# Kernel optimization log

Hardware: AMD Instinct MI355X
Metric: run time of the kernel (lower is better)

The kernel has to match this reference:

```python
import jax, jax.numpy as jnp
import numpy as np

B, T, D = 2, 2048, 2048
H = 16
NOPE, ROPE = 128, 64
Q_HEAD = NOPE + ROPE            # 192
Q_LORA = H * Q_HEAD // 4        # 768
KV_RANK = 512
V_DIM = 128
EPS = 1e-6


def setup_inputs() -> dict:
    key = jax.random.key(0)
    ks = jax.random.split(key, 8)
    s = lambda k, shape: jax.random.normal(k, shape, dtype=jnp.float32) * (1.0 / np.sqrt(shape[0]))
    return {
        "hidden_states": jax.random.normal(ks[0], (B, T, D), dtype=jnp.float32),
        "positions": jnp.broadcast_to(jnp.arange(T, dtype=jnp.int64 if jax.config.jax_enable_x64 else jnp.int32), (B, T)),
        "w_qa": s(ks[1], (D, Q_LORA)),
        "g_qa": jnp.ones((Q_LORA,), jnp.float32),
        "w_qb": s(ks[2], (Q_LORA, H * Q_HEAD)),
        "w_kva": s(ks[3], (D, KV_RANK + ROPE)),
        "g_kva": jnp.ones((KV_RANK,), jnp.float32),
        "w_kvb": s(ks[4], (KV_RANK, H * (NOPE + V_DIM))),
        "w_o": s(ks[5], (H * V_DIM, D)),
    }


def _rms(x, g):
    return x * jax.lax.rsqrt(jnp.mean(x * x, axis=-1, keepdims=True) + EPS) * g


def _rotate_half(x):
    h = x.shape[-1] // 2
    return jnp.concatenate([-x[..., h:], x[..., :h]], axis=-1)


def _rope_tables(n):
    inv_freq = 1.0 / (10000.0 ** (jnp.arange(0, ROPE, 2, dtype=jnp.float32) / ROPE))
    freqs = jnp.arange(n, dtype=jnp.float32)[:, None] * inv_freq[None, :]
    emb = jnp.concatenate([freqs, freqs], axis=-1)  # [n, ROPE]
    return jnp.cos(emb), jnp.sin(emb)


def reference(hidden_states, positions, w_qa, g_qa, w_qb, w_kva, g_kva, w_kvb, w_o):
    Bq, Tq, _ = hidden_states.shape
    # Q: low-rank down-proj + RMSNorm + up-proj
    q = _rms(hidden_states @ w_qa, g_qa) @ w_qb
    q = q.reshape(Bq, Tq, H, Q_HEAD)
    q_nope, q_rope = q[..., :NOPE], q[..., NOPE:]
    # KV compression (prefill: no past cache, S == T)
    kvc = hidden_states @ w_kva
    new_c_kv = _rms(kvc[..., :KV_RANK], g_kva)     # [B,S,rank]
    new_k_rope = kvc[..., KV_RANK:]                # [B,S,ROPE]
    S = new_c_kv.shape[1]
    kv = (new_c_kv @ w_kvb).reshape(Bq, S, H, NOPE + V_DIM)
    k_nope, v = kv[..., :NOPE], kv[..., NOPE:]
    # Decoupled RoPE on the rope sub-dimension only
    cos_full, sin_full = _rope_tables(S)
    cos_q = cos_full[positions][:, :, None, :]     # [B,T,1,ROPE]
    sin_q = sin_full[positions][:, :, None, :]
    q_rope = q_rope * cos_q + _rotate_half(q_rope) * sin_q
    cos_k = cos_full[None, :, :]                   # [1,S,ROPE] (all_positions = arange(S))
    sin_k = sin_full[None, :, :]
    k_rope = new_k_rope * cos_k + _rotate_half(new_k_rope) * sin_k  # [B,S,ROPE], shared across heads
    # Assemble full q/k, attention
    q_full = jnp.concatenate([q_nope, q_rope], axis=-1).transpose(0, 2, 1, 3)  # [B,H,T,192]
    k_full = jnp.concatenate(
        [k_nope, jnp.broadcast_to(k_rope[:, :, None, :], (Bq, S, H, ROPE))], axis=-1
    ).transpose(0, 2, 1, 3)                                                     # [B,H,S,192]
    v = v.transpose(0, 2, 1, 3)                                                 # [B,H,S,Vd]
    scale = Q_HEAD ** -0.5
    attn = jnp.einsum("bhtd,bhsd->bhts", q_full, k_full) * scale
    row = jnp.arange(Tq)[:, None]
    col = jnp.arange(S)[None, :]
    attn = jnp.where(col > row + (S - Tq), -jnp.inf, attn)
    attn = jax.nn.softmax(attn, axis=-1)
    out = jnp.einsum("bhts,bhsd->bhtd", attn, v)
    out = out.transpose(0, 2, 1, 3).reshape(Bq, Tq, H * V_DIM)
    output = out @ w_o
    return output, new_c_kv, new_k_rope
```

## Files before the change

kernel.cpp:

```cpp
#include <hip/hip_runtime.h>
#include <stdint.h>

typedef unsigned short ushort_t;
typedef ushort_t u16x8 __attribute__((ext_vector_type(8)));
typedef short s16x8 __attribute__((ext_vector_type(8)));
typedef float f32x4 __attribute__((ext_vector_type(4)));

#define B_ 2
#define T_ 2048
#define D_ 2048
#define H_ 16
#define NOPE_ 128
#define ROPE_ 64
#define QHEAD_ 192
#define QLORA_ 768
#define KVRANK_ 512
#define VDIM_ 128
#define MROWS (B_*T_)
#define QKVW 1408

#define MAGIC_F32  0x3F800000u
#define MAGIC_BF16 0x3F803F80u

#define QK_SCALE 0.07216878364870323f

__device__ __forceinline__ float bf2f(ushort_t u) {
    return __uint_as_float(((uint32_t)u) << 16);
}
__device__ __forceinline__ ushort_t f2bf(float f) {
    uint32_t x = __float_as_uint(f);
    x += 0x7fffu + ((x >> 16) & 1u);
    return (ushort_t)(x >> 16);
}

__device__ __forceinline__ void async_ld16(const ushort_t* g, ushort_t* l) {
    __builtin_amdgcn_global_load_lds(
        (const __attribute__((address_space(1))) void*)g,
        (__attribute__((address_space(3))) void*)l, 16, 0, 0);
}

__launch_bounds__(256)
__global__ void gemm_mfma(const ushort_t* __restrict__ A,
                          const ushort_t* __restrict__ BT,
                          float* __restrict__ C, int M, int N, int K) {
    __shared__ ushort_t As[128 * 32];
    __shared__ ushort_t Bs[128 * 32];

    const int tid = threadIdx.x;
    const int lane = tid & 63;
    const int n16 = lane & 15, quad = lane >> 4;
    const int m0 = blockIdx.y * 128, n0 = blockIdx.x * 128;
    const int w = tid >> 6;
    const int wm = (w & 1) * 64, wn = (w >> 1) * 64;

    f32x4 acc[4][4];
#pragma unroll
    for (int i = 0; i < 4; i++)
#pragma unroll
        for (int j = 0; j < 4; j++) acc[i][j] = (f32x4){0.f, 0.f, 0.f, 0.f};

    const int wbase = tid & ~63;
    for (int kt = 0; kt < K; kt += 32) {
        __syncthreads();
#pragma unroll
        for (int iss = 0; iss < 2; iss++) {
            const int chunk = iss * 256 + tid;
            const int row = chunk >> 2, col = (chunk & 3) * 8;
            const int lbase = (iss * 256 + wbase) * 8;
            async_ld16(A + (long)(m0 + row) * K + kt + col, &As[lbase]);
            async_ld16(BT + (long)(n0 + row) * K + kt + col, &Bs[lbase]);
        }
        __syncthreads();

        s16x8 af[4], bf[4];
#pragma unroll
        for (int i = 0; i < 4; i++) {
            af[i] = *(const s16x8*)&As[(wm + i * 16 + n16) * 32 + quad * 8];
            bf[i] = *(const s16x8*)&Bs[(wn + i * 16 + n16) * 32 + quad * 8];
        }
#pragma unroll
        for (int i = 0; i < 4; i++)
#pragma unroll
            for (int j = 0; j < 4; j++)
                acc[i][j] = __builtin_amdgcn_mfma_f32_16x16x32_bf16(af[i], bf[j], acc[i][j], 0, 0, 0);
    }

#pragma unroll
    for (int i = 0; i < 4; i++) {
        const long mrow = m0 + wm + i * 16 + quad * 4;
#pragma unroll
        for (int j = 0; j < 4; j++) {
            const int nc = n0 + wn + j * 16 + n16;
#pragma unroll
            for (int r = 0; r < 4; r++)
                C[(mrow + r) * N + nc] = acc[i][j][r];
        }
    }
}

__launch_bounds__(256)
__global__ void gemm_mfma_h(const ushort_t* __restrict__ A,
                            const ushort_t* __restrict__ BT,
                            ushort_t* __restrict__ C, int M, int N, int K) {
    __shared__ ushort_t As[128 * 32];
    __shared__ ushort_t Bs[128 * 32];

    const int tid = threadIdx.x;
    const int lane = tid & 63;
    const int n16 = lane & 15, quad = lane >> 4;
    const int m0 = blockIdx.y * 128, n0 = blockIdx.x * 128;
    const int w = tid >> 6;
    const int wm = (w & 1) * 64, wn = (w >> 1) * 64;

    f32x4 acc[4][4];
#pragma unroll
    for (int i = 0; i < 4; i++)
#pragma unroll
        for (int j = 0; j < 4; j++) acc[i][j] = (f32x4){0.f, 0.f, 0.f, 0.f};

    const int wbase = tid & ~63;
    for (int kt = 0; kt < K; kt += 32) {
        __syncthreads();
#pragma unroll
        for (int iss = 0; iss < 2; iss++) {
            const int chunk = iss * 256 + tid;
            const int row = chunk >> 2, col = (chunk & 3) * 8;
            const int lbase = (iss * 256 + wbase) * 8;
            async_ld16(A + (long)(m0 + row) * K + kt + col, &As[lbase]);
            async_ld16(BT + (long)(n0 + row) * K + kt + col, &Bs[lbase]);
        }
        __syncthreads();

        s16x8 af[4], bf[4];
#pragma unroll
        for (int i = 0; i < 4; i++) {
            af[i] = *(const s16x8*)&As[(wm + i * 16 + n16) * 32 + quad * 8];
            bf[i] = *(const s16x8*)&Bs[(wn + i * 16 + n16) * 32 + quad * 8];
        }
#pragma unroll
        for (int i = 0; i < 4; i++)
#pragma unroll
            for (int j = 0; j < 4; j++)
                acc[i][j] = __builtin_amdgcn_mfma_f32_16x16x32_bf16(af[i], bf[j], acc[i][j], 0, 0, 0);
    }

#pragma unroll
    for (int i = 0; i < 4; i++) {
        const long mrow = m0 + wm + i * 16 + quad * 4;
#pragma unroll
        for (int j = 0; j < 4; j++) {
            const int nc = n0 + wn + j * 16 + n16;
#pragma unroll
            for (int r = 0; r < 4; r++)
                C[(mrow + r) * N + nc] = f2bf(acc[i][j][r]);
        }
    }
}

__launch_bounds__(256)
__global__ void gemm_out_k(const uint32_t* __restrict__ probe,
                           const ushort_t* __restrict__ A,
                           const ushort_t* __restrict__ BT,
                           float* __restrict__ Cf, ushort_t* __restrict__ Ch,
                           int M, int N, int K) {
    __shared__ ushort_t As[128 * 32];
    __shared__ ushort_t Bs[128 * 32];

    const bool isf = (*probe == MAGIC_F32);
    const int tid = threadIdx.x;
    const int lane = tid & 63;
    const int n16 = lane & 15, quad = lane >> 4;
    const int m0 = blockIdx.y * 128, n0 = blockIdx.x * 128;
    const int w = tid >> 6;
    const int wm = (w & 1) * 64, wn = (w >> 1) * 64;

    f32x4 acc[4][4];
#pragma unroll
    for (int i = 0; i < 4; i++)
#pragma unroll
        for (int j = 0; j < 4; j++) acc[i][j] = (f32x4){0.f, 0.f, 0.f, 0.f};

    const int wbase = tid & ~63;
    for (int kt = 0; kt < K; kt += 32) {
        __syncthreads();
#pragma unroll
        for (int iss = 0; iss < 2; iss++) {
            const int chunk = iss * 256 + tid;
            const int row = chunk >> 2, col = (chunk & 3) * 8;
            const int lbase = (iss * 256 + wbase) * 8;
            async_ld16(A + (long)(m0 + row) * K + kt + col, &As[lbase]);
            async_ld16(BT + (long)(n0 + row) * K + kt + col, &Bs[lbase]);
        }
        __syncthreads();

        s16x8 af[4], bf[4];
#pragma unroll
        for (int i = 0; i < 4; i++) {
            af[i] = *(const s16x8*)&As[(wm + i * 16 + n16) * 32 + quad * 8];
            bf[i] = *(const s16x8*)&Bs[(wn + i * 16 + n16) * 32 + quad * 8];
        }
#pragma unroll
        for (int i = 0; i < 4; i++)
#pragma unroll
            for (int j = 0; j < 4; j++)
                acc[i][j] = __builtin_amdgcn_mfma_f32_16x16x32_bf16(af[i], bf[j], acc[i][j], 0, 0, 0);
    }

#pragma unroll
    for (int i = 0; i < 4; i++) {
        const long mrow = m0 + wm + i * 16 + quad * 4;
#pragma unroll
        for (int j = 0; j < 4; j++) {
            const int nc = n0 + wn + j * 16 + n16;
            if (isf) {
#pragma unroll
                for (int r = 0; r < 4; r++)
                    Cf[(mrow + r) * N + nc] = acc[i][j][r];
            } else {
#pragma unroll
                for (int r = 0; r < 4; r++)
                    Ch[(mrow + r) * N + nc] = f2bf(acc[i][j][r]);
            }
        }
    }
}

__launch_bounds__(256)
__global__ void gemm_kv_k(const ushort_t* __restrict__ A,
                          const ushort_t* __restrict__ BT,
                          ushort_t* __restrict__ kvK,
                          ushort_t* __restrict__ vTm,
                          int M, int N, int K) {
    __shared__ ushort_t As[128 * 32];
    __shared__ ushort_t Bs[128 * 32];

    const int tid = threadIdx.x;
    const int lane = tid & 63;
    const int n16 = lane & 15, quad = lane >> 4;
    const int m0 = blockIdx.y * 128, n0 = blockIdx.x * 128;
    const int w = tid >> 6;
    const int wm = (w & 1) * 64, wn = (w >> 1) * 64;

    f32x4 acc[4][4];
#pragma unroll
    for (int i = 0; i < 4; i++)
#pragma unroll
        for (int j = 0; j < 4; j++) acc[i][j] = (f32x4){0.f, 0.f, 0.f, 0.f};

    const int wbase = tid & ~63;
    for (int kt = 0; kt < K; kt += 32) {
        __syncthreads();
#pragma unroll
        for (int iss = 0; iss < 2; iss++) {
            const int chunk = iss * 256 + tid;
            const int row = chunk >> 2, col = (chunk & 3) * 8;
            const int lbase = (iss * 256 + wbase) * 8;
            async_ld16(A + (long)(m0 + row) * K + kt + col, &As[lbase]);
            async_ld16(BT + (long)(n0 + row) * K + kt + col, &Bs[lbase]);
        }
        __syncthreads();

        s16x8 af[4], bf[4];
#pragma unroll
        for (int i = 0; i < 4; i++) {
            af[i] = *(const s16x8*)&As[(wm + i * 16 + n16) * 32 + quad * 8];
            bf[i] = *(const s16x8*)&Bs[(wn + i * 16 + n16) * 32 + quad * 8];
        }
#pragma unroll
        for (int i = 0; i < 4; i++)
#pragma unroll
            for (int j = 0; j < 4; j++)
                acc[i][j] = __builtin_amdgcn_mfma_f32_16x16x32_bf16(af[i], bf[j], acc[i][j], 0, 0, 0);
    }

    const bool isV = (n0 & 128) != 0;
#pragma unroll
    for (int i = 0; i < 4; i++) {
        const long mrowb = m0 + wm + i * 16 + quad * 4;
#pragma unroll
        for (int j = 0; j < 4; j++) {
            const int nc = n0 + wn + j * 16 + n16;
            const int hh = nc >> 8, dd = nc & 127;
            if (!isV) {
#pragma unroll
                for (int r = 0; r < 4; r++)
                    kvK[(mrowb + r) * (H_ * NOPE_) + hh * NOPE_ + dd] = f2bf(acc[i][j][r]);
            } else {
#pragma unroll
                for (int r = 0; r < 4; r++) {
                    const long mrow = mrowb + r;
                    const long bb = mrow >> 11, ss = mrow & (T_ - 1);
                    vTm[((bb * H_ + hh) * VDIM_ + dd) * (long)T_ + ss] = f2bf(acc[i][j][r]);
                }
            }
        }
    }
}

__launch_bounds__(256)
__global__ void cvt_trans_k(const uint32_t* __restrict__ probe,
                            const float* __restrict__ srcf,
                            const ushort_t* __restrict__ srch,
                            ushort_t* __restrict__ dst,
                            int K, int N, int NP, float scl) {
    const bool isf = (*probe == MAGIC_F32);
    __shared__ float tile[32][33];
    const int kb = blockIdx.y * 32, nb = blockIdx.x * 32;
    const int tx = threadIdx.x & 31, ty = threadIdx.x >> 5;
#pragma unroll
    for (int i = 0; i < 32; i += 8) {
        const int n = nb + tx;
        const long idx = (long)(kb + ty + i) * N + n;
        tile[ty + i][tx] = (n < N) ? (isf ? srcf[idx] : bf2f(srch[idx])) : 0.f;
    }
    __syncthreads();
#pragma unroll
    for (int i = 0; i < 32; i += 8) {
        const int n = nb + ty + i;
        if (n < NP) dst[(long)n * K + kb + tx] = f2bf(tile[tx][ty + i] * scl);
    }
}

__launch_bounds__(256)
__global__ void cvt_copy_k(const uint32_t* __restrict__ probe,
                           const float* __restrict__ srcf,
                           const ushort_t* __restrict__ srch,
                           ushort_t* __restrict__ dst, long n) {
    const bool isf = (*probe == MAGIC_F32);
    const long i = ((long)blockIdx.x * 256 + threadIdx.x) * 8;
    if (i + 8 <= n) {
        u16x8 o;
        if (isf) {
            float4 a = *(const float4*)(srcf + i);
            float4 b = *(const float4*)(srcf + i + 4);
            o[0]=f2bf(a.x); o[1]=f2bf(a.y); o[2]=f2bf(a.z); o[3]=f2bf(a.w);
            o[4]=f2bf(b.x); o[5]=f2bf(b.y); o[6]=f2bf(b.z); o[7]=f2bf(b.w);
        } else {
            o = *(const u16x8*)(srch + i);
        }
        *(u16x8*)(dst + i) = o;
    }
}

__launch_bounds__(256)
__global__ void rms12rope_k(const uint32_t* __restrict__ probe,
                            const float* __restrict__ qkv,
                            const float* __restrict__ g1f, const ushort_t* __restrict__ g1h,
                            const float* __restrict__ g2f, const ushort_t* __restrict__ g2h,
                            ushort_t* __restrict__ qln,
                            float* __restrict__ ockf, ushort_t* __restrict__ ockh,
                            ushort_t* __restrict__ ckv_i,
                            float* __restrict__ okrf, ushort_t* __restrict__ okrh,
                            ushort_t* __restrict__ krope_rot) {
    const bool isf = (*probe == MAGIC_F32);
    const int row = blockIdx.x;
    const int tid = threadIdx.x;
    const float* ir = qkv + (long)row * QKVW;

    float s1 = 0.f, s2 = 0.f;
    for (int c = tid; c < QLORA_; c += 256) { float x = ir[c]; s1 += x * x; }
    for (int c = tid; c < KVRANK_; c += 256) { float x = ir[QLORA_ + c]; s2 += x * x; }
    __shared__ float r1[256], r2[256];
    r1[tid] = s1; r2[tid] = s2;
    __syncthreads();
    for (int s = 128; s > 0; s >>= 1) {
        if (tid < s) { r1[tid] += r1[tid + s]; r2[tid] += r2[tid + s]; }
        __syncthreads();
    }
    const float inv1 = rsqrtf(r1[0] / (float)QLORA_ + 1e-6f);
    const float inv2 = rsqrtf(r2[0] / (float)KVRANK_ + 1e-6f);

    for (int c = tid; c < QLORA_; c += 256)
        qln[(long)row * QLORA_ + c] = f2bf(ir[c] * inv1 * (isf ? g1f[c] : bf2f(g1h[c])));
    for (int c = tid; c < KVRANK_; c += 256) {
        const float v = ir[QLORA_ + c] * inv2 * (isf ? g2f[c] : bf2f(g2h[c]));
        if (isf) ockf[(long)row * KVRANK_ + c] = v;
        else     ockh[(long)row * KVRANK_ + c] = f2bf(v);
        ckv_i[(long)row * KVRANK_ + c] = f2bf(v);
    }

    if (tid < 64) {
        const int lane = tid;
        const int t = row & (T_ - 1);
        const float x = ir[QLORA_ + KVRANK_ + lane];
        const float other = ir[QLORA_ + KVRANK_ + (lane ^ 32)];
        const int fi = lane & 31;
        const float inv_freq = exp2f((float)fi * (-13.287712379549449f / 32.f));
        const float ang = (float)t * inv_freq;
        float sn, cs;
        sincosf(ang, &sn, &cs);
        const float rot = (lane < 32) ? -other : other;
        if (isf) okrf[(long)row * ROPE_ + lane] = x;
        else     okrh[(long)row * ROPE_ + lane] = f2bf(x);
        krope_rot[(long)row * ROPE_ + lane] = f2bf(x * cs + rot * sn);
    }
}

__launch_bounds__(256)
__global__ void rope_q_k(ushort_t* __restrict__ q) {
    const int w = threadIdx.x >> 6, lane = threadIdx.x & 63;
    const int idx = blockIdx.x * 4 + w;
    const int h = idx & (H_ - 1);
    const int row = idx >> 4;
    const int t = row & (T_ - 1);
    ushort_t* qr = q + (long)row * (H_ * QHEAD_) + h * QHEAD_ + NOPE_;

    const float x = bf2f(qr[lane]);
    const float other = bf2f(qr[lane ^ 32]);
    const int fi = lane & 31;
    const float inv_freq = exp2f((float)fi * (-13.287712379549449f / 32.f));
    const float ang = (float)t * inv_freq;
    float sn, cs;
    sincosf(ang, &sn, &cs);
    const float rot = (lane < 32) ? -other : other;
    qr[lane] = f2bf(x * cs + rot * sn);
}

#define BQ 64
#define BK 64
#define PSTR 68

__launch_bounds__(256, 2)
__global__ void attn_mfma_k(const ushort_t* __restrict__ q,
                            const ushort_t* __restrict__ kvK,
                            const ushort_t* __restrict__ vTm,
                            const ushort_t* __restrict__ krope,
                            ushort_t* __restrict__ attn_out) {
    __shared__ ushort_t ks[2][BK * 192];
    __shared__ ushort_t ps[4][16][PSTR];

    const int tid = threadIdx.x;
    const int w = tid >> 6, lane = tid & 63;
    const int n16 = lane & 15, quad = lane >> 4;

    const int L = (int)blockIdx.x;
    const int slot = L >> 3;
    const int bhg = slot >> 5;
    const int qts = slot & 31;
    const int bh = (L & 7) | (bhg << 3);
    const int qt = (bhg & 1) ? (31 - qts) : qts;
    const int h = bh & (H_ - 1), b = bh >> 4;

    const int q0 = qt * BQ;
    const int qw = q0 + w * 16;

    s16x8 qf[6];
    {
        const ushort_t* qrow = q + (long)(b * T_ + qw + n16) * (H_ * QHEAD_) + h * QHEAD_;
#pragma unroll
        for (int c = 0; c < 6; c++)
            qf[c] = *(const s16x8*)(qrow + c * 32 + quad * 8);
    }

    s16x8 kones;
#pragma unroll
    for (int j = 0; j < 8; j++) kones[j] = (short)0x3F80;

    f32x4 O[8];
#pragma unroll
    for (int f = 0; f < 8; f++) O[f] = (f32x4){0.f, 0.f, 0.f, 0.f};
    float mrow[4], lrow[4];
#pragma unroll
    for (int r = 0; r < 4; r++) { mrow[r] = -3.0e38f; lrow[r] = 0.f; }

    const int ntiles = qt + 1;

    const ushort_t* spb[6];  int sstr[6];
#pragma unroll
    for (int i = 0; i < 6; i++) {
        const int off = w * 6144 + i * 1024 + lane * 16;
        const int row = off / 384;
        const int c16 = (off % 384) >> 4;
        const int csrc = c16 ^ (row & 7);
        if (csrc < 16) {
            spb[i] = kvK + (long)(b * T_ + row) * (H_ * NOPE_) + h * NOPE_ + csrc * 8;
            sstr[i] = H_ * NOPE_;
        } else {
            spb[i] = krope + (long)(b * T_ + row) * ROPE_ + (csrc - 16) * 8;
            sstr[i] = ROPE_;
        }
    }

    const ushort_t* vbase = vTm + ((long)bh * VDIM_ + n16) * T_ + quad * 8;
    const int r7 = n16 & 7;

#pragma unroll
    for (int i = 0; i < 6; i++)
        async_ld16(spb[i], &ks[0][w * 3072 + i * 512]);

    int cur = 0;
    for (int kt = 0; kt < ntiles; kt++) {
        const int s0 = kt * BK;
        const int sn = (kt + 1 < ntiles ? kt + 1 : kt) * BK;

        s16x8 vb[2][8];
#pragma unroll
        for (int kc = 0; kc < 2; kc++)
#pragma unroll
            for (int vt = 0; vt < 8; vt++)
                vb[kc][vt] = *(const s16x8*)(vbase + (long)(vt * 16) * T_ + s0 + kc * 32);
        __builtin_amdgcn_sched_barrier(0);

        asm volatile("s_waitcnt vmcnt(16)" ::: "memory");
        __builtin_amdgcn_s_barrier();
        __builtin_amdgcn_sched_barrier(0);

#pragma unroll
        for (int i = 0; i < 6; i++)
            async_ld16(spb[i] + (long)sn * sstr[i], &ks[cur ^ 1][w * 3072 + i * 512]);
        __builtin_amdgcn_sched_barrier(0);

        const ushort_t* kb = &ks[cur][0];
        f32x4 Sc[4];
        __builtin_amdgcn_s_setprio(1);
#pragma unroll
        for (int st = 0; st < 4; st++) {
            Sc[st] = (f32x4){0.f, 0.f, 0.f, 0.f};
            const int row = st * 16 + n16;
            const int rbase = row * 192;
#pragma unroll
            for (int c = 0; c < 4; c++) {
                s16x8 bfr = *(const s16x8*)&kb[rbase + (((4 * c + quad) ^ r7) << 3)];
                Sc[st] = __builtin_amdgcn_mfma_f32_16x16x32_bf16(qf[c], bfr, Sc[st], 0, 0, 0);
            }
#pragma unroll
            for (int c2 = 0; c2 < 2; c2++) {
                s16x8 bfr = *(const s16x8*)&kb[rbase + (((16 + 4 * c2 + quad) ^ r7) << 3)];
                Sc[st] = __builtin_amdgcn_mfma_f32_16x16x32_bf16(qf[4 + c2], bfr, Sc[st], 0, 0, 0);
            }
        }
        __builtin_amdgcn_s_setprio(0);

        const bool diag = (s0 + BK > q0);
        float Sv[4][4];
#pragma unroll
        for (int st = 0; st < 4; st++) {
            const int sg = s0 + st * 16 + n16;
#pragma unroll
            for (int r = 0; r < 4; r++) {
                float v = Sc[st][r];
                if (diag && sg > qw + quad * 4 + r) v = -3.0e38f;
                Sv[st][r] = v;
            }
        }

        float rmx[4];
#pragma unroll
        for (int r = 0; r < 4; r++)
            rmx[r] = fmaxf(fmaxf(Sv[0][r], Sv[1][r]), fmaxf(Sv[2][r], Sv[3][r]));

        bool ok = true;
#pragma unroll
        for (int r = 0; r < 4; r++) ok = ok && (rmx[r] <= mrow[r] + 8.0f);
        if (!__all(ok)) {
            float mnew[4], alpha[4];
#pragma unroll
            for (int r = 0; r < 4; r++) {
                float mx = rmx[r];
#pragma unroll
                for (int off = 8; off > 0; off >>= 1)
                    mx = fmaxf(mx, __shfl_xor(mx, off, 64));
                mnew[r] = fmaxf(mrow[r], mx);
                alpha[r] = __expf(mrow[r] - mnew[r]);
                mrow[r] = mnew[r];
                lrow[r] *= alpha[r];
            }
#pragma unroll
            for (int f = 0; f < 8; f++)
#pragma unroll
                for (int r = 0; r < 4; r++) O[f][r] *= alpha[r];
        }

#pragma unroll
        for (int st = 0; st < 4; st++)
#pragma unroll
            for (int r = 0; r < 4; r++)
                ps[w][quad * 4 + r][st * 16 + n16] = f2bf(__expf(Sv[st][r] - mrow[r]));

        asm volatile("s_waitcnt vmcnt(6)" ::: "memory");
        __builtin_amdgcn_sched_barrier(0);

        f32x4 sacc = (f32x4){0.f, 0.f, 0.f, 0.f};
        __builtin_amdgcn_s_setprio(1);
#pragma unroll
        for (int kc = 0; kc < 2; kc++) {
            s16x8 afr = *(const s16x8*)&ps[w][n16][kc * 32 + quad * 8];
            sacc = __builtin_amdgcn_mfma_f32_16x16x32_bf16(afr, kones, sacc, 0, 0, 0);
#pragma unroll
            for (int vt = 0; vt < 8; vt++)
                O[vt] = __builtin_amdgcn_mfma_f32_16x16x32_bf16(afr, vb[kc][vt], O[vt], 0, 0, 0);
        }
        __builtin_amdgcn_s_setprio(0);
#pragma unroll
        for (int r = 0; r < 4; r++) lrow[r] += sacc[r];

        cur ^= 1;
    }

    float linv[4];
#pragma unroll
    for (int r = 0; r < 4; r++) linv[r] = 1.f / lrow[r];
    ushort_t* obase = attn_out + (long)(b * T_ + qw) * (H_ * VDIM_) + h * VDIM_;
#pragma unroll
    for (int vt = 0; vt < 8; vt++)
#pragma unroll
        for (int r = 0; r < 4; r++)
            obase[(long)(quad * 4 + r) * (H_ * VDIM_) + vt * 16 + n16] =
                f2bf(O[vt][r] * linv[r]);
}

extern "C" void kernel_launch(void* const* d_in, const int* in_sizes, int n_in,
                              void* d_out, int out_size, void* d_ws, size_t ws_size,
                              hipStream_t stream) {
    const uint32_t* probe = (const uint32_t*)d_in[3];

    char* ws = (char*)d_ws;
    ushort_t* q      = (ushort_t*)ws;
    ushort_t* hs_b   = (ushort_t*)ws;
    ushort_t* woT    = (ushort_t*)ws;
    ushort_t* kvK    = (ushort_t*)(ws + 25165824);
    ushort_t* vTm    = (ushort_t*)(ws + 41943040);
    float*    qkv    = (float*)(ws + 25165824);
    ushort_t* wqaT   = (ushort_t*)(ws + 48234496);
    ushort_t* wkvaT  = (ushort_t*)(ws + 51380224);
    ushort_t* wqbT   = (ushort_t*)(ws + 48234496);
    ushort_t* attn_i = (ushort_t*)(ws + 58720256);
    ushort_t* ckv_i  = (ushort_t*)(ws + 58720256);
    ushort_t* qln    = (ushort_t*)(ws + 62914560);
    ushort_t* wkvbT  = (ushort_t*)(ws + 69206016);
    ushort_t* krope  = (ushort_t*)(ws + 76283904 - 786432);

    const float* hs_f  = (const float*)d_in[0];
    const float* wqa_f = (const float*)d_in[2];
    const float* gqa_f = (const float*)d_in[3];
    const float* wqb_f = (const float*)d_in[4];
    const float* wkva_f= (const float*)d_in[5];
    const float* gkva_f= (const float*)d_in[6];
    const float* wkvb_f= (const float*)d_in[7];
    const float* wo_f  = (const float*)d_in[8];
    float* oy_f  = (float*)d_out;
    float* ock_f = oy_f + (long)MROWS * D_;
    float* okr_f = ock_f + (long)MROWS * KVRANK_;

    const ushort_t* hs_h  = (const ushort_t*)d_in[0];
    const ushort_t* wqa_h = (const ushort_t*)d_in[2];
    const ushort_t* gqa_h = (const ushort_t*)d_in[3];
    const ushort_t* wqb_h = (const ushort_t*)d_in[4];
    const ushort_t* wkva_h= (const ushort_t*)d_in[5];
    const ushort_t* gkva_h= (const ushort_t*)d_in[6];
    const ushort_t* wkvb_h= (const ushort_t*)d_in[7];
    const ushort_t* wo_h  = (const ushort_t*)d_in[8];
    ushort_t* oy_h  = (ushort_t*)d_out;
    ushort_t* ock_h = oy_h + (long)MROWS * D_;
    ushort_t* okr_h = ock_h + (long)MROWS * KVRANK_;

    const dim3 blk(256);

    cvt_copy_k<<<4096, blk, 0, stream>>>(probe, hs_f, hs_h, hs_b, (long)MROWS * D_);
    cvt_trans_k<<<dim3(24, 64), blk, 0, stream>>>(probe, wqa_f, wqa_h, wqaT, D_, QLORA_, QLORA_, 1.f);
    cvt_trans_k<<<dim3(20, 64), blk, 0, stream>>>(probe, wkva_f, wkva_h, wkvaT, D_, KVRANK_ + ROPE_, 640, 1.f);

    gemm_mfma<<<dim3(QKVW / 128, MROWS / 128), blk, 0, stream>>>(hs_b, wqaT, qkv, MROWS, QKVW, D_);

    rms12rope_k<<<MROWS, blk, 0, stream>>>(probe, qkv, gqa_f, gqa_h, gkva_f, gkva_h,
                                           qln, ock_f, ock_h, ckv_i, okr_f, okr_h, krope);

    cvt_trans_k<<<dim3(96, 24), blk, 0, stream>>>(probe, wqb_f, wqb_h, wqbT, QLORA_, H_ * QHEAD_, H_ * QHEAD_, QK_SCALE);
    gemm_mfma_h<<<dim3((H_ * QHEAD_) / 128, MROWS / 128), blk, 0, stream>>>(qln, wqbT, q, MROWS, H_ * QHEAD_, QLORA_);

    cvt_trans_k<<<dim3(128, 16), blk, 0, stream>>>(probe, wkvb_f, wkvb_h, wkvbT, KVRANK_, H_ * 256, H_ * 256, 1.f);
    gemm_kv_k<<<dim3((H_ * 256) / 128, MROWS / 128), blk, 0, stream>>>(ckv_i, wkvbT, kvK, vTm, MROWS, H_ * 256, KVRANK_);

    rope_q_k<<<(MROWS * H_) / 4, blk, 0, stream>>>(q);
    attn_mfma_k<<<dim3(B_ * H_ * (T_ / BQ)), blk, 0, stream>>>(q, kvK, vTm, krope, attn_i);

    cvt_trans_k<<<dim3(64, 64), blk, 0, stream>>>(probe, wo_f, wo_h, woT, H_ * VDIM_, D_, D_, 1.f);
    gemm_out_k<<<dim3(D_ / 128, MROWS / 128), blk, 0, stream>>>(probe, attn_i, woT, oy_f, oy_h, MROWS, D_, H_ * VDIM_);
}
```

Before: 526.3 us.

## Fuse Q RoPE into attention, use exp2 softmax, XCD-swizzle GEMM tiles, stage V transpose

```diff
diff --git a/kernel.cpp b/kernel.cpp
--- a/kernel.cpp
+++ b/kernel.cpp
@@ -22,7 +22,8 @@
 #define MAGIC_F32  0x3F800000u
 #define MAGIC_BF16 0x3F803F80u
 
-#define QK_SCALE 0.07216878364870323f
+#define QK_SCALE2 0.10411754851533622f
+#define DEFER_THR 11.5415603271117f
 
 __device__ __forceinline__ float bf2f(ushort_t u) {
     return __uint_as_float(((uint32_t)u) << 16);
@@ -37,6 +38,15 @@
     __builtin_amdgcn_global_load_lds(
         (const __attribute__((address_space(1))) void*)g,
         (__attribute__((address_space(3))) void*)l, 16, 0, 0);
+}
+
+__device__ __forceinline__ void xcd_tile(int& m0, int& n0) {
+    const int nx = gridDim.x;
+    const int nwg = nx * gridDim.y;
+    int lin = (int)blockIdx.y * nx + (int)blockIdx.x;
+    lin = (lin & 7) * (nwg >> 3) + (lin >> 3);
+    n0 = (lin % nx) * 128;
+    m0 = (lin / nx) * 128;
 }
 
 __launch_bounds__(256)
@@ -49,7 +59,8 @@
     const int tid = threadIdx.x;
     const int lane = tid & 63;
     const int n16 = lane & 15, quad = lane >> 4;
-    const int m0 = blockIdx.y * 128, n0 = blockIdx.x * 128;
+    int m0, n0;
+    xcd_tile(m0, n0);
     const int w = tid >> 6;
     const int wm = (w & 1) * 64, wn = (w >> 1) * 64;
 
@@ -108,7 +119,8 @@
     const int tid = threadIdx.x;
     const int lane = tid & 63;
     const int n16 = lane & 15, quad = lane >> 4;
-    const int m0 = blockIdx.y * 128, n0 = blockIdx.x * 128;
+    int m0, n0;
+    xcd_tile(m0, n0);
     const int w = tid >> 6;
     const int wm = (w & 1) * 64, wn = (w >> 1) * 64;
 
@@ -170,7 +182,8 @@
     const int tid = threadIdx.x;
     const int lane = tid & 63;
     const int n16 = lane & 15, quad = lane >> 4;
-    const int m0 = blockIdx.y * 128, n0 = blockIdx.x * 128;
+    int m0, n0;
+    xcd_tile(m0, n0);
     const int w = tid >> 6;
     const int wm = (w & 1) * 64, wn = (w >> 1) * 64;
 
@@ -237,7 +250,8 @@
     const int tid = threadIdx.x;
     const int lane = tid & 63;
     const int n16 = lane & 15, quad = lane >> 4;
-    const int m0 = blockIdx.y * 128, n0 = blockIdx.x * 128;
+    int m0, n0;
+    xcd_tile(m0, n0);
     const int w = tid >> 6;
     const int wm = (w & 1) * 64, wn = (w >> 1) * 64;
 
@@ -274,25 +288,40 @@
     }
 
     const bool isV = (n0 & 128) != 0;
-#pragma unroll
-    for (int i = 0; i < 4; i++) {
-        const long mrowb = m0 + wm + i * 16 + quad * 4;
-#pragma unroll
-        for (int j = 0; j < 4; j++) {
-            const int nc = n0 + wn + j * 16 + n16;
-            const int hh = nc >> 8, dd = nc & 127;
-            if (!isV) {
+    if (!isV) {
+#pragma unroll
+        for (int i = 0; i < 4; i++) {
+            const long mrowb = m0 + wm + i * 16 + quad * 4;
+#pragma unroll
+            for (int j = 0; j < 4; j++) {
+                const int nc = n0 + wn + j * 16 + n16;
+                const int hh = nc >> 8, dd = nc & 127;
 #pragma unroll
                 for (int r = 0; r < 4; r++)
                     kvK[(mrowb + r) * (H_ * NOPE_) + hh * NOPE_ + dd] = f2bf(acc[i][j][r]);
-            } else {
-#pragma unroll
-                for (int r = 0; r < 4; r++) {
-                    const long mrow = mrowb + r;
-                    const long bb = mrow >> 11, ss = mrow & (T_ - 1);
-                    vTm[((bb * H_ + hh) * VDIM_ + dd) * (long)T_ + ss] = f2bf(acc[i][j][r]);
-                }
             }
+        }
+    } else {
+        __syncthreads();
+        ushort_t* tb = (w < 2) ? &As[w * 1152] : &Bs[(w - 2) * 1152];
+        const int hh  = (n0 + wn) >> 8;
+        const long bb = (long)((m0 + wm) >> 11);
+        const int ssb = (m0 + wm) & (T_ - 1);
+        const int ddb = (n0 + wn) & 127;
+        const int ddr = lane >> 2;
+        const int c0  = (lane & 3) * 16;
+#pragma unroll
+        for (int j = 0; j < 4; j++) {
+#pragma unroll
+            for (int i = 0; i < 4; i++)
+#pragma unroll
+                for (int r = 0; r < 4; r++)
+                    tb[n16 * 72 + i * 16 + quad * 4 + r] = f2bf(acc[i][j][r]);
+            u16x8 v0 = *(const u16x8*)&tb[ddr * 72 + c0];
+            u16x8 v1 = *(const u16x8*)&tb[ddr * 72 + c0 + 8];
+            ushort_t* dstp = vTm + ((bb * H_ + hh) * VDIM_ + ddb + j * 16 + ddr) * (long)T_ + ssb + c0;
+            *(u16x8*)dstp = v0;
+            *(u16x8*)(dstp + 8) = v1;
         }
     }
 }
@@ -396,26 +425,6 @@
     }
 }
 
-__launch_bounds__(256)
-__global__ void rope_q_k(ushort_t* __restrict__ q) {
-    const int w = threadIdx.x >> 6, lane = threadIdx.x & 63;
-    const int idx = blockIdx.x * 4 + w;
-    const int h = idx & (H_ - 1);
-    const int row = idx >> 4;
-    const int t = row & (T_ - 1);
-    ushort_t* qr = q + (long)row * (H_ * QHEAD_) + h * QHEAD_ + NOPE_;
-
-    const float x = bf2f(qr[lane]);
-    const float other = bf2f(qr[lane ^ 32]);
-    const int fi = lane & 31;
-    const float inv_freq = exp2f((float)fi * (-13.287712379549449f / 32.f));
-    const float ang = (float)t * inv_freq;
-    float sn, cs;
-    sincosf(ang, &sn, &cs);
-    const float rot = (lane < 32) ? -other : other;
-    qr[lane] = f2bf(x * cs + rot * sn);
-}
-
 #define BQ 64
 #define BK 64
 #define PSTR 68
@@ -450,6 +459,20 @@
 #pragma unroll
         for (int c = 0; c < 6; c++)
             qf[c] = *(const s16x8*)(qrow + c * 32 + quad * 8);
+    }
+    {
+        const int t = qw + n16;
+#pragma unroll
+        for (int j = 0; j < 8; j++) {
+            const int d = quad * 8 + j;
+            const float inv_freq = exp2f((float)d * (-13.287712379549449f / 32.f));
+            float sn, cs;
+            sincosf((float)t * inv_freq, &sn, &cs);
+            const float x0 = bf2f((ushort_t)qf[4][j]);
+            const float x1 = bf2f((ushort_t)qf[5][j]);
+            qf[4][j] = (short)f2bf(x0 * cs - x1 * sn);
+            qf[5][j] = (short)f2bf(x1 * cs + x0 * sn);
+        }
     }
 
     s16x8 kones;
@@ -551,7 +574,7 @@
 
         bool ok = true;
 #pragma unroll
-        for (int r = 0; r < 4; r++) ok = ok && (rmx[r] <= mrow[r] + 8.0f);
+        for (int r = 0; r < 4; r++) ok = ok && (rmx[r] <= mrow[r] + DEFER_THR);
         if (!__all(ok)) {
             float mnew[4], alpha[4];
 #pragma unroll
@@ -561,7 +584,7 @@
                 for (int off = 8; off > 0; off >>= 1)
                     mx = fmaxf(mx, __shfl_xor(mx, off, 64));
                 mnew[r] = fmaxf(mrow[r], mx);
-                alpha[r] = __expf(mrow[r] - mnew[r]);
+                alpha[r] = exp2f(mrow[r] - mnew[r]);
                 mrow[r] = mnew[r];
                 lrow[r] *= alpha[r];
             }
@@ -575,7 +598,7 @@
         for (int st = 0; st < 4; st++)
 #pragma unroll
             for (int r = 0; r < 4; r++)
-                ps[w][quad * 4 + r][st * 16 + n16] = f2bf(__expf(Sv[st][r] - mrow[r]));
+                ps[w][quad * 4 + r][st * 16 + n16] = f2bf(exp2f(Sv[st][r] - mrow[r]));
 
         asm volatile("s_waitcnt vmcnt(6)" ::: "memory");
         __builtin_amdgcn_sched_barrier(0);
@@ -665,13 +688,12 @@
     rms12rope_k<<<MROWS, blk, 0, stream>>>(probe, qkv, gqa_f, gqa_h, gkva_f, gkva_h,
                                            qln, ock_f, ock_h, ckv_i, okr_f, okr_h, krope);
 
-    cvt_trans_k<<<dim3(96, 24), blk, 0, stream>>>(probe, wqb_f, wqb_h, wqbT, QLORA_, H_ * QHEAD_, H_ * QHEAD_, QK_SCALE);
+    cvt_trans_k<<<dim3(96, 24), blk, 0, stream>>>(probe, wqb_f, wqb_h, wqbT, QLORA_, H_ * QHEAD_, H_ * QHEAD_, QK_SCALE2);
     gemm_mfma_h<<<dim3((H_ * QHEAD_) / 128, MROWS / 128), blk, 0, stream>>>(qln, wqbT, q, MROWS, H_ * QHEAD_, QLORA_);
 
     cvt_trans_k<<<dim3(128, 16), blk, 0, stream>>>(probe, wkvb_f, wkvb_h, wkvbT, KVRANK_, H_ * 256, H_ * 256, 1.f);
     gemm_kv_k<<<dim3((H_ * 256) / 128, MROWS / 128), blk, 0, stream>>>(ckv_i, wkvbT, kvK, vTm, MROWS, H_ * 256, KVRANK_);
 
-    rope_q_k<<<(MROWS * H_) / 4, blk, 0, stream>>>(q);
     attn_mfma_k<<<dim3(B_ * H_ * (T_ / BQ)), blk, 0, stream>>>(q, kvK, vTm, krope, attn_i);
 
     cvt_trans_k<<<dim3(64, 64), blk, 0, stream>>>(probe, wo_f, wo_h, woT, H_ * VDIM_, D_, D_, 1.f);
```

Result: faster. 506.8 us (median of 3 runs) (-3.7%).
